# Kernel optimization log

Measured on AMD Instinct MI355X. Metric: run time of the kernel, lower is better.

The kernel has to match this reference:

```python
import jax, jax.numpy as jnp
import numpy as np

M_FACTORS = [12, 8, 8]
N_FACTORS = [8, 8, 12]
E = 4          # hardcoded in original: gates.view(B, 4, 1, 1, 1)
R = 8          # TT rank
ALPHA = 16.0   # common_alpha
TAU = 1.0


def setup_inputs() -> dict:
    key = jax.random.key(0)
    ks = jax.random.split(key, 11)
    B, S, m = 32, 512, 768
    inp = {
        "X": jax.random.normal(ks[0], (B, S, m), jnp.float32),
        "router_w": jax.random.normal(ks[1], (E, m), jnp.float32) * 0.02,
        "router_b": jax.random.normal(ks[2], (E,), jnp.float32) * 0.02,
        "base_w": jax.random.normal(ks[3], (m, m), jnp.float32) * 0.02,
        "base_b": jax.random.normal(ks[4], (m,), jnp.float32) * 0.02,
        "core0": jax.random.normal(ks[5], (E, 1, 12, R), jnp.float32) * 0.1,
        "core1": jax.random.normal(ks[6], (E, R, 8, R), jnp.float32) * 0.1,
        "core2": jax.random.normal(ks[7], (E, R, 8, R), jnp.float32) * 0.1,
        "core3": jax.random.normal(ks[8], (E, R, 8, R), jnp.float32) * 0.1,
        "core4": jax.random.normal(ks[9], (E, R, 8, R), jnp.float32) * 0.1,
        "core5": jax.random.normal(ks[10], (E, R, 12, 1), jnp.float32) * 0.1,
    }
    return inp


def _gumbel_softmax_hard(logits, key):
    # torch.nn.functional.gumbel_softmax(logits, tau=TAU, hard=True)
    u = jax.random.uniform(key, logits.shape, logits.dtype, 1e-6, 1.0 - 1e-6)
    g = -jnp.log(-jnp.log(u))
    y_soft = jax.nn.softmax((logits + g) / TAU, axis=-1)
    y_hard = jax.nn.one_hot(jnp.argmax(y_soft, axis=-1), logits.shape[-1],
                            dtype=logits.dtype)
    # straight-through: y_hard - sg(y_soft) + y_soft
    return jax.lax.stop_gradient(y_hard - y_soft) + y_soft


def _tt_moe(X, gates, cores):
    # faithful to tensorized_multiplication_experts
    B, S, m = X.shape
    # [B, 1, S, m_factors[::-1]] -> last axis is m_factors[0]
    tt_state = X.reshape([B, 1, S] + M_FACTORS[::-1])
    num_m = len(M_FACTORS)
    for i in range(num_m):
        # per-sample expert-weighted core: [B, r, f, p]
        mc = jnp.einsum('be,erfp->brfp', gates, cores[i])
        tt_state = jnp.einsum('br...m,brmp->bp...', tt_state, mc)
    for i in range(len(N_FACTORS)):
        mc = jnp.einsum('be,erfp->brfp', gates, cores[num_m + i])
        tt_state = jnp.einsum('br...,brnp->bp...n', tt_state, mc)
    return tt_state.reshape(B, S, -1)  # trailing p == 1


def reference(X, router_w, router_b, base_w, base_b,
              core0, core1, core2, core3, core4, core5):
    cores = [core0, core1, core2, core3, core4, core5]
    pooled = X.mean(axis=1)                              # [B, m]
    logits = pooled @ router_w.T + router_b              # [B, E]
    gates = _gumbel_softmax_hard(logits, jax.random.key(42))
    base_out = X @ base_w.T + base_b                     # F.linear
    Z = _tt_moe(X, gates, cores)                         # [B, S, n]
    return Z * ALPHA + base_out
```

## Files before the change

kernel.cpp:

```cpp
#include <hip/hip_runtime.h>
#include <hip/hip_bf16.h>
#include <stdint.h>

#define GAS __attribute__((address_space(1)))
#define LAS __attribute__((address_space(3)))

typedef __attribute__((ext_vector_type(8))) short bf16x8;
typedef __attribute__((ext_vector_type(4))) float f32x4;

struct us4 { unsigned short x, y, z, w; };

__device__ __forceinline__ void gl_lds16(const void* g, void* lds) {
  __builtin_amdgcn_global_load_lds((const GAS unsigned int*)(uintptr_t)g,
                                   (LAS unsigned int*)(uintptr_t)lds, 16, 0, 0);
}

__device__ __forceinline__ unsigned short f2bf(float f) {
  unsigned u = __float_as_uint(f);
  return (unsigned short)((u + 0x7fffu + ((u >> 16) & 1u)) >> 16);
}

__device__ __forceinline__ void threefry2x32_42(unsigned x0, unsigned x1,
                                                unsigned* o0, unsigned* o1) {
  const unsigned k0 = 0u, k1 = 42u;
  unsigned ks[3] = {k0, k1, k0 ^ k1 ^ 0x1BD11BDAu};
  x0 += ks[0]; x1 += ks[1];
  const int rot[2][4] = {{13, 15, 26, 6}, {17, 29, 16, 24}};
#pragma unroll
  for (int i = 0; i < 5; ++i) {
#pragma unroll
    for (int j = 0; j < 4; ++j) {
      int r = rot[i & 1][j];
      x0 += x1;
      x1 = (x1 << r) | (x1 >> (32 - r));
      x1 ^= x0;
    }
    x0 += ks[(i + 1) % 3];
    x1 += ks[(i + 2) % 3] + (unsigned)(i + 1);
  }
  *o0 = x0; *o1 = x1;
}

__global__ __launch_bounds__(256) void k_prep(
    const float* __restrict__ X, const float* __restrict__ rw,
    const float* __restrict__ bw,
    const float* __restrict__ c0, const float* __restrict__ c1,
    const float* __restrict__ c2, const float* __restrict__ c3,
    const float* __restrict__ c4, const float* __restrict__ c5,
    unsigned short* __restrict__ Xbf, float* __restrict__ partial,
    unsigned short* __restrict__ Wbt) {
  __shared__ __align__(16) char smem[31232];
  int t = threadIdx.x;
  int bid = blockIdx.x;

  if (bid < 192) {
    int e = bid / 48, jc = bid % 48;
    float* KA = (float*)smem;
    float* LB = (float*)(smem + 3072);
    float* Kt = (float*)(smem + 6144);
    float* LtS = (float*)(smem + 30720);
    for (int q = t; q < 768; q += 256) {
      int bc = q >> 3, p2 = q & 7;
      int b2 = bc / 12, cc = bc % 12;
      float s = 0.f;
#pragma unroll
      for (int p1 = 0; p1 < 8; ++p1)
        s += c0[e * 96 + cc * 8 + p1] * c1[((e * 8 + p1) * 8 + b2) * 8 + p2];
      KA[q] = s;
      int p4 = q / 96, mm = q % 96;
      int n2 = mm / 12, n3 = mm % 12;
      float s2 = 0.f;
#pragma unroll
      for (int p5 = 0; p5 < 8; ++p5)
        s2 += c4[((e * 8 + p4) * 8 + n2) * 8 + p5] * c5[(e * 8 + p5) * 12 + n3];
      LB[q] = s2;
    }
    __syncthreads();
    for (int q = t; q < 6144; q += 256) {
      int i = q >> 3, p3 = q & 7;
      int a = i / 96, bc = i % 96;
      float s = 0.f;
#pragma unroll
      for (int p2 = 0; p2 < 8; ++p2)
        s += KA[bc * 8 + p2] * c2[((e * 8 + p2) * 8 + a) * 8 + p3];
      Kt[p3 * 768 + i] = s;
    }
    if (t < 128) {
      int i = t >> 3, p3 = t & 7;
      int j = jc * 16 + i;
      int n1 = j / 96, mm = j % 96;
      float s2 = 0.f;
#pragma unroll
      for (int p4 = 0; p4 < 8; ++p4)
        s2 += c3[((e * 8 + p3) * 8 + n1) * 8 + p4] * LB[p4 * 96 + mm];
      LtS[i * 8 + p3] = s2;
    }
    __syncthreads();
    for (int idx = t; idx < 12288; idx += 256) {
      int jl = idx / 768, i = idx - jl * 768;
      int j = jc * 16 + jl;
      float s = 0.f;
#pragma unroll
      for (int p = 0; p < 8; ++p) s += Kt[p * 768 + i] * LtS[jl * 8 + p];
      float val = bw[(size_t)j * 768 + i] + 16.0f * s;
      Wbt[(size_t)e * 589824 + (size_t)j * 768 + i] = f2bf(val);
    }
  } else {
    float* red = (float*)smem;
    int p = bid - 192;
    int r0 = p * 32;
    float lp0 = 0.f, lp1 = 0.f, lp2 = 0.f, lp3 = 0.f;
    if (t < 192) {
      const float* xp = X + (size_t)r0 * 768 + t * 4;
      unsigned short* xo = Xbf + (size_t)r0 * 768 + t * 4;
      float4 acc = {0.f, 0.f, 0.f, 0.f};
#pragma unroll 8
      for (int r = 0; r < 32; ++r) {
        float4 v = *reinterpret_cast<const float4*>(xp + (size_t)r * 768);
        acc.x += v.x; acc.y += v.y; acc.z += v.z; acc.w += v.w;
        us4 o;
        o.x = f2bf(v.x); o.y = f2bf(v.y); o.z = f2bf(v.z); o.w = f2bf(v.w);
        *reinterpret_cast<us4*>(xo + (size_t)r * 768) = o;
      }
      float4 w0 = *reinterpret_cast<const float4*>(rw + 0 * 768 + t * 4);
      float4 w1 = *reinterpret_cast<const float4*>(rw + 1 * 768 + t * 4);
      float4 w2 = *reinterpret_cast<const float4*>(rw + 2 * 768 + t * 4);
      float4 w3 = *reinterpret_cast<const float4*>(rw + 3 * 768 + t * 4);
      lp0 = acc.x * w0.x + acc.y * w0.y + acc.z * w0.z + acc.w * w0.w;
      lp1 = acc.x * w1.x + acc.y * w1.y + acc.z * w1.z + acc.w * w1.w;
      lp2 = acc.x * w2.x + acc.y * w2.y + acc.z * w2.z + acc.w * w2.w;
      lp3 = acc.x * w3.x + acc.y * w3.y + acc.z * w3.z + acc.w * w3.w;
    }
#pragma unroll
    for (int off = 32; off > 0; off >>= 1) {
      lp0 += __shfl_down(lp0, off);
      lp1 += __shfl_down(lp1, off);
      lp2 += __shfl_down(lp2, off);
      lp3 += __shfl_down(lp3, off);
    }
    int w = t >> 6;
    if ((t & 63) == 0 && w < 3) {
      red[w * 4 + 0] = lp0; red[w * 4 + 1] = lp1;
      red[w * 4 + 2] = lp2; red[w * 4 + 3] = lp3;
    }
    __syncthreads();
    if (t < 4) partial[p * 4 + t] = red[0 + t] + red[4 + t] + red[8 + t];
  }
}

__global__ __launch_bounds__(256, 4) void k_gemm(
    const unsigned short* __restrict__ Xbf,
    const unsigned short* __restrict__ Wbt,
    const float* __restrict__ partial,
    const float* __restrict__ rb,
    const float* __restrict__ base_b,
    float* __restrict__ out)
{
  __shared__ unsigned short sA[128 * 64];
  __shared__ unsigned short sB[128 * 64];
  int t = threadIdx.x;
  int w = t >> 6, l = t & 63;
  int l16 = l & 15, l4 = l >> 4;

  int bid = blockIdx.x;
  int work = (bid & 7) * 96 + (bid >> 3);
  int mtile = work / 6, ntile = work - mtile * 6;
  int m0 = mtile * 128, n0 = ntile * 128;
  int b = mtile >> 2;

  int bi = 0;
  {
    float v = -1e30f;
    if (l < 4) {
      float s = 0.f;
#pragma unroll
      for (int c = 0; c < 16; ++c) s += partial[(b * 16 + c) * 4 + l];
      float lg = s * (1.0f / 512.0f) + rb[l];
      int idx = b * 4 + l;
      unsigned x0, x1;
      threefry2x32_42(0u, (unsigned)idx, &x0, &x1);
      unsigned bits = x0 ^ x1;
      float u01 = __uint_as_float((bits >> 9) | 0x3f800000u) - 1.0f;
      float u = u01 * ((1.0f - 1e-6f) - 1e-6f) + 1e-6f;
      u = fmaxf(u, 1e-6f);
      v = lg + (-logf(-logf(u)));
      bi = l;
#pragma unroll
      for (int off = 1; off < 4; off <<= 1) {
        float vo = __shfl_xor(v, off);
        int io = __shfl_xor(bi, off);
        if (vo > v || (vo == v && io < bi)) { v = vo; bi = io; }
      }
    }
    bi = __shfl(bi, 0);
  }
  const unsigned short* Wb = Wbt + (size_t)bi * 589824;
  int wr = w >> 1, wc = w & 1;

  f32x4 acc[4][4];
#pragma unroll
  for (int i = 0; i < 4; ++i)
#pragma unroll
    for (int jj = 0; jj < 4; ++jj) acc[i][jj] = (f32x4)0.f;

  int rows[4], csw[4];
#pragma unroll
  for (int q = 0; q < 4; ++q) {
    int ci = (w * 4 + q) * 64 + l;
    rows[q] = ci >> 3;
    csw[q] = ((ci & 7) * 8) ^ ((rows[q] & 7) << 3);
  }

  int xorr = (l16 & 7) << 3;
  for (int k0 = 0; k0 < 768; k0 += 64) {
#pragma unroll
    for (int q = 0; q < 4; ++q) {
      const unsigned short* ga = Xbf + (size_t)(m0 + rows[q]) * 768 + k0 + csw[q];
      gl_lds16(ga, &sA[(w * 4 + q) * 512]);
      const unsigned short* gb = Wb + (size_t)(n0 + rows[q]) * 768 + k0 + csw[q];
      gl_lds16(gb, &sB[(w * 4 + q) * 512]);
    }
    __syncthreads();
#pragma unroll
    for (int kk = 0; kk < 2; ++kk) {
      int coff = (kk * 32 + l4 * 8) ^ xorr;
      bf16x8 af[4], bfr[4];
#pragma unroll
      for (int am = 0; am < 4; ++am)
        af[am] = *reinterpret_cast<const bf16x8*>(
            &sA[(wr * 64 + am * 16 + l16) * 64 + coff]);
#pragma unroll
      for (int bn = 0; bn < 4; ++bn)
        bfr[bn] = *reinterpret_cast<const bf16x8*>(
            &sB[(wc * 64 + bn * 16 + l16) * 64 + coff]);
#pragma unroll
      for (int am = 0; am < 4; ++am)
#pragma unroll
        for (int bn = 0; bn < 4; ++bn)
          acc[am][bn] = __builtin_amdgcn_mfma_f32_16x16x32_bf16(
              bfr[bn], af[am], acc[am][bn], 0, 0, 0);
    }
    __syncthreads();
  }

  f32x4 bb4[4];
#pragma unroll
  for (int bn = 0; bn < 4; ++bn)
    bb4[bn] = *reinterpret_cast<const f32x4*>(base_b + n0 + wc * 64 + bn * 16 + l4 * 4);
#pragma unroll
  for (int am = 0; am < 4; ++am) {
    int m = m0 + wr * 64 + am * 16 + l16;
    float* op = out + (size_t)m * 768 + n0 + wc * 64 + l4 * 4;
#pragma unroll
    for (int bn = 0; bn < 4; ++bn) {
      f32x4 v = acc[am][bn] + bb4[bn];
      *reinterpret_cast<f32x4*>(op + bn * 16) = v;
    }
  }
}

extern "C" void kernel_launch(void* const* d_in, const int* in_sizes, int n_in,
                              void* d_out, int out_size, void* d_ws, size_t ws_size,
                              hipStream_t stream) {
  const float* X  = (const float*)d_in[0];
  const float* rw = (const float*)d_in[1];
  const float* rb = (const float*)d_in[2];
  const float* bw = (const float*)d_in[3];
  const float* bb = (const float*)d_in[4];
  const float* c0 = (const float*)d_in[5];
  const float* c1 = (const float*)d_in[6];
  const float* c2 = (const float*)d_in[7];
  const float* c3 = (const float*)d_in[8];
  const float* c4 = (const float*)d_in[9];
  const float* c5 = (const float*)d_in[10];
  float* out = (float*)d_out;

  char* ws = (char*)d_ws;
  float* partial      = (float*)(ws + 4096);
  unsigned short* Wbt = (unsigned short*)(ws + 262144);
  unsigned short* Xbf = (unsigned short*)(ws + 4980736);

  k_prep<<<704, 256, 0, stream>>>(X, rw, bw, c0, c1, c2, c3, c4, c5,
                                  Xbf, partial, Wbt);
  k_gemm<<<768, 256, 0, stream>>>(Xbf, Wbt, partial, rb, bb, out);
}
```

Before: 56.41 us.

## Fuse X fp32-to-bf16 conversion into GEMM A-tile loading with register prefetch

Drops the separate bf16 copy of X written by the prep kernel. The GEMM now reads fp32 X directly, converts it to bf16 in registers and writes it into swizzled LDS. The next A tile is prefetched into registers while the MFMAs run, and the B tile is still staged through global_load_lds. This removes the Xbf write and re-read traffic, but doubles the bytes of A the GEMM reads, adds register pressure under launch_bounds(256,4), and adds an extra barrier per k-step.

```diff
diff --git a/kernel.cpp b/kernel.cpp
--- a/kernel.cpp
+++ b/kernel.cpp
@@ -47,8 +47,7 @@
     const float* __restrict__ c0, const float* __restrict__ c1,
     const float* __restrict__ c2, const float* __restrict__ c3,
     const float* __restrict__ c4, const float* __restrict__ c5,
-    unsigned short* __restrict__ Xbf, float* __restrict__ partial,
-    unsigned short* __restrict__ Wbt) {
+    float* __restrict__ partial, unsigned short* __restrict__ Wbt) {
   __shared__ __align__(16) char smem[31232];
   int t = threadIdx.x;
   int bid = blockIdx.x;
@@ -112,15 +111,11 @@
     float lp0 = 0.f, lp1 = 0.f, lp2 = 0.f, lp3 = 0.f;
     if (t < 192) {
       const float* xp = X + (size_t)r0 * 768 + t * 4;
-      unsigned short* xo = Xbf + (size_t)r0 * 768 + t * 4;
       float4 acc = {0.f, 0.f, 0.f, 0.f};
 #pragma unroll 8
       for (int r = 0; r < 32; ++r) {
         float4 v = *reinterpret_cast<const float4*>(xp + (size_t)r * 768);
         acc.x += v.x; acc.y += v.y; acc.z += v.z; acc.w += v.w;
-        us4 o;
-        o.x = f2bf(v.x); o.y = f2bf(v.y); o.z = f2bf(v.z); o.w = f2bf(v.w);
-        *reinterpret_cast<us4*>(xo + (size_t)r * 768) = o;
       }
       float4 w0 = *reinterpret_cast<const float4*>(rw + 0 * 768 + t * 4);
       float4 w1 = *reinterpret_cast<const float4*>(rw + 1 * 768 + t * 4);
@@ -149,7 +144,7 @@
 }
 
 __global__ __launch_bounds__(256, 4) void k_gemm(
-    const unsigned short* __restrict__ Xbf,
+    const float* __restrict__ X,
     const unsigned short* __restrict__ Wbt,
     const float* __restrict__ partial,
     const float* __restrict__ rb,
@@ -203,24 +198,55 @@
 #pragma unroll
     for (int jj = 0; jj < 4; ++jj) acc[i][jj] = (f32x4)0.f;
 
-  int rows[4], csw[4];
+  int arow[4], agc[4], adst[4], csw[4];
 #pragma unroll
   for (int q = 0; q < 4; ++q) {
     int ci = (w * 4 + q) * 64 + l;
-    rows[q] = ci >> 3;
-    csw[q] = ((ci & 7) * 8) ^ ((rows[q] & 7) << 3);
-  }
+    int row = ci >> 3, slot = ci & 7;
+    arow[q] = row;
+    agc[q] = slot * 8;
+    adst[q] = row * 64 + (slot ^ (row & 7)) * 8;
+    csw[q] = agc[q] ^ ((row & 7) << 3);
+  }
+
+#define A_LOAD(av, k0)                                                         \
+  _Pragma("unroll") for (int q = 0; q < 4; ++q) {                              \
+    const float* ap = X + (size_t)(m0 + arow[q]) * 768 + (k0) + agc[q];        \
+    av[q][0] = *reinterpret_cast<const f32x4*>(ap);                            \
+    av[q][1] = *reinterpret_cast<const f32x4*>(ap + 4);                        \
+  }
+#define A_CVT(av, ab)                                                          \
+  _Pragma("unroll") for (int q = 0; q < 4; ++q) {                              \
+    _Pragma("unroll") for (int j = 0; j < 4; ++j) {                            \
+      ab[q][j] = (short)f2bf(av[q][0][j]);                                     \
+      ab[q][j + 4] = (short)f2bf(av[q][1][j]);                                 \
+    }                                                                          \
+  }
+#define A_WRITE(ab)                                                            \
+  _Pragma("unroll") for (int q = 0; q < 4; ++q)                                \
+    *reinterpret_cast<bf16x8*>(&sA[adst[q]]) = ab[q];
+#define B_STAGE(k0)                                                            \
+  _Pragma("unroll") for (int q = 0; q < 4; ++q) {                              \
+    const unsigned short* gb =                                                 \
+        Wb + (size_t)(n0 + arow[q]) * 768 + (k0) + csw[q];                     \
+    gl_lds16(gb, &sB[(w * 4 + q) * 512]);                                      \
+  }
+
+  {
+    f32x4 av[4][2];
+    bf16x8 ab[4];
+    A_LOAD(av, 0);
+    A_CVT(av, ab);
+    A_WRITE(ab);
+    B_STAGE(0);
+  }
+  __syncthreads();
 
   int xorr = (l16 & 7) << 3;
-  for (int k0 = 0; k0 < 768; k0 += 64) {
-#pragma unroll
-    for (int q = 0; q < 4; ++q) {
-      const unsigned short* ga = Xbf + (size_t)(m0 + rows[q]) * 768 + k0 + csw[q];
-      gl_lds16(ga, &sA[(w * 4 + q) * 512]);
-      const unsigned short* gb = Wb + (size_t)(n0 + rows[q]) * 768 + k0 + csw[q];
-      gl_lds16(gb, &sB[(w * 4 + q) * 512]);
-    }
-    __syncthreads();
+  for (int kt = 0; kt < 12; ++kt) {
+    f32x4 av[4][2];
+    bf16x8 ab[4];
+    if (kt < 11) A_LOAD(av, (kt + 1) * 64);
 #pragma unroll
     for (int kk = 0; kk < 2; ++kk) {
       int coff = (kk * 32 + l4 * 8) ^ xorr;
@@ -240,8 +266,18 @@
           acc[am][bn] = __builtin_amdgcn_mfma_f32_16x16x32_bf16(
               bfr[bn], af[am], acc[am][bn], 0, 0, 0);
     }
+    if (kt < 11) A_CVT(av, ab);
     __syncthreads();
-  }
+    if (kt < 11) {
+      A_WRITE(ab);
+      B_STAGE((kt + 1) * 64);
+      __syncthreads();
+    }
+  }
+#undef A_LOAD
+#undef A_CVT
+#undef A_WRITE
+#undef B_STAGE
 
   f32x4 bb4[4];
 #pragma unroll
@@ -278,9 +314,8 @@
   char* ws = (char*)d_ws;
   float* partial      = (float*)(ws + 4096);
   unsigned short* Wbt = (unsigned short*)(ws + 262144);
-  unsigned short* Xbf = (unsigned short*)(ws + 4980736);
 
   k_prep<<<704, 256, 0, stream>>>(X, rw, bw, c0, c1, c2, c3, c4, c5,
-                                  Xbf, partial, Wbt);
-  k_gemm<<<768, 256, 0, stream>>>(Xbf, Wbt, partial, rb, bb, out);
-}
+                                  partial, Wbt);
+  k_gemm<<<768, 256, 0, stream>>>(X, Wbt, partial, rb, bb, out);
+}
```

After: 91.93 us. +63.0%, slower.

## Fuse X bf16 conversion into GEMM A-tile loads, drop Xbf staging buffer

Applied to the files above, without the earlier changes.

Removes the separate fp32-to-bf16 conversion of X in the prep kernel and the write and re-read of the bf16 copy. The GEMM now loads fp32 X tiles straight into LDS with a swizzled layout and converts to bf16 when building MFMA fragments. This saves the Xbf global write and reread, but doubles the A-tile LDS footprint and global load bytes per tile. It also adds conversion ALU work in the inner loop, and each X tile is converted once per N-tile (6 times) instead of once overall. Occupancy launch bound is relaxed.

```diff
diff --git a/kernel.cpp b/kernel.cpp
--- a/kernel.cpp
+++ b/kernel.cpp
@@ -47,8 +47,7 @@
     const float* __restrict__ c0, const float* __restrict__ c1,
     const float* __restrict__ c2, const float* __restrict__ c3,
     const float* __restrict__ c4, const float* __restrict__ c5,
-    unsigned short* __restrict__ Xbf, float* __restrict__ partial,
-    unsigned short* __restrict__ Wbt) {
+    float* __restrict__ partial, unsigned short* __restrict__ Wbt) {
   __shared__ __align__(16) char smem[31232];
   int t = threadIdx.x;
   int bid = blockIdx.x;
@@ -112,15 +111,11 @@
     float lp0 = 0.f, lp1 = 0.f, lp2 = 0.f, lp3 = 0.f;
     if (t < 192) {
       const float* xp = X + (size_t)r0 * 768 + t * 4;
-      unsigned short* xo = Xbf + (size_t)r0 * 768 + t * 4;
       float4 acc = {0.f, 0.f, 0.f, 0.f};
 #pragma unroll 8
       for (int r = 0; r < 32; ++r) {
         float4 v = *reinterpret_cast<const float4*>(xp + (size_t)r * 768);
         acc.x += v.x; acc.y += v.y; acc.z += v.z; acc.w += v.w;
-        us4 o;
-        o.x = f2bf(v.x); o.y = f2bf(v.y); o.z = f2bf(v.z); o.w = f2bf(v.w);
-        *reinterpret_cast<us4*>(xo + (size_t)r * 768) = o;
       }
       float4 w0 = *reinterpret_cast<const float4*>(rw + 0 * 768 + t * 4);
       float4 w1 = *reinterpret_cast<const float4*>(rw + 1 * 768 + t * 4);
@@ -148,15 +143,15 @@
   }
 }
 
-__global__ __launch_bounds__(256, 4) void k_gemm(
-    const unsigned short* __restrict__ Xbf,
+__global__ __launch_bounds__(256) void k_gemm(
+    const float* __restrict__ X,
     const unsigned short* __restrict__ Wbt,
     const float* __restrict__ partial,
     const float* __restrict__ rb,
     const float* __restrict__ base_b,
     float* __restrict__ out)
 {
-  __shared__ unsigned short sA[128 * 64];
+  __shared__ float sAf[128 * 64];
   __shared__ unsigned short sB[128 * 64];
   int t = threadIdx.x;
   int w = t >> 6, l = t & 63;
@@ -203,21 +198,32 @@
 #pragma unroll
     for (int jj = 0; jj < 4; ++jj) acc[i][jj] = (f32x4)0.f;
 
-  int rows[4], csw[4];
+  int arowq[8], acolq[8];
+#pragma unroll
+  for (int q = 0; q < 8; ++q) {
+    int ci = (w * 8 + q) * 64 + l;
+    int row = ci >> 4, slot = ci & 15;
+    arowq[q] = row;
+    acolq[q] = (((slot >> 1) ^ (row & 7)) << 3) + ((slot & 1) << 2);
+  }
+  int brow[4], bcsw[4];
 #pragma unroll
   for (int q = 0; q < 4; ++q) {
     int ci = (w * 4 + q) * 64 + l;
-    rows[q] = ci >> 3;
-    csw[q] = ((ci & 7) * 8) ^ ((rows[q] & 7) << 3);
+    brow[q] = ci >> 3;
+    bcsw[q] = ((ci & 7) * 8) ^ ((brow[q] & 7) << 3);
   }
 
   int xorr = (l16 & 7) << 3;
   for (int k0 = 0; k0 < 768; k0 += 64) {
 #pragma unroll
+    for (int q = 0; q < 8; ++q) {
+      const float* ga = X + (size_t)(m0 + arowq[q]) * 768 + k0 + acolq[q];
+      gl_lds16(ga, &sAf[((w * 8 + q) * 64 + l) * 4]);
+    }
+#pragma unroll
     for (int q = 0; q < 4; ++q) {
-      const unsigned short* ga = Xbf + (size_t)(m0 + rows[q]) * 768 + k0 + csw[q];
-      gl_lds16(ga, &sA[(w * 4 + q) * 512]);
-      const unsigned short* gb = Wb + (size_t)(n0 + rows[q]) * 768 + k0 + csw[q];
+      const unsigned short* gb = Wb + (size_t)(n0 + brow[q]) * 768 + k0 + bcsw[q];
       gl_lds16(gb, &sB[(w * 4 + q) * 512]);
     }
     __syncthreads();
@@ -226,9 +232,20 @@
       int coff = (kk * 32 + l4 * 8) ^ xorr;
       bf16x8 af[4], bfr[4];
 #pragma unroll
-      for (int am = 0; am < 4; ++am)
-        af[am] = *reinterpret_cast<const bf16x8*>(
-            &sA[(wr * 64 + am * 16 + l16) * 64 + coff]);
+      for (int am = 0; am < 4; ++am) {
+        int r = wr * 64 + am * 16 + l16;
+        int g = (kk * 4 + l4) ^ (r & 7);
+        const float* ap = &sAf[r * 64 + g * 8];
+        f32x4 a0 = *reinterpret_cast<const f32x4*>(ap);
+        f32x4 a1 = *reinterpret_cast<const f32x4*>(ap + 4);
+        bf16x8 v;
+#pragma unroll
+        for (int j = 0; j < 4; ++j) {
+          v[j] = (short)f2bf(a0[j]);
+          v[j + 4] = (short)f2bf(a1[j]);
+        }
+        af[am] = v;
+      }
 #pragma unroll
       for (int bn = 0; bn < 4; ++bn)
         bfr[bn] = *reinterpret_cast<const bf16x8*>(
@@ -278,9 +295,8 @@
   char* ws = (char*)d_ws;
   float* partial      = (float*)(ws + 4096);
   unsigned short* Wbt = (unsigned short*)(ws + 262144);
-  unsigned short* Xbf = (unsigned short*)(ws + 4980736);
 
   k_prep<<<704, 256, 0, stream>>>(X, rw, bw, c0, c1, c2, c3, c4, c5,
-                                  Xbf, partial, Wbt);
-  k_gemm<<<768, 256, 0, stream>>>(Xbf, Wbt, partial, rb, bb, out);
-}
+                                  partial, Wbt);
+  k_gemm<<<768, 256, 0, stream>>>(X, Wbt, partial, rb, bb, out);
+}
```

Result: slower. 63.19 us (+12.0%).
